# Kernel optimization log

Measured on AMD Instinct MI355X. Metric: run time of the kernel, lower is better.

Reference implementation:

```python
import jax, jax.numpy as jnp
import numpy as np

B, E = 8, 4096  # batch, embedding_size


def setup_inputs() -> dict:
    key = jax.random.key(0)
    k0, k1, k2, k3, k4 = jax.random.split(key, 5)
    return {
        "input": jax.random.normal(k0, (B, E), dtype=jnp.float32),
        "yin": jax.random.normal(k1, (B, E), dtype=jnp.float32),
        "hebb": jax.random.normal(k2, (E, E), dtype=jnp.float32),
        # learned parameters (match torch init: 0.01*randn / 0.01*ones)
        "w": 0.01 * jax.random.normal(k3, (E, E), dtype=jnp.float32),
        "alpha": 0.01 * jax.random.normal(k4, (E, E), dtype=jnp.float32),
        "eta": 0.01 * jnp.ones((1,), dtype=jnp.float32),
    }


def reference(input, yin, hebb, w, alpha, eta):
    # hebbian plasticity forward:
    # yout = tanh(yin @ (w + alpha * hebb) + input)            [B, E]
    yout = jnp.tanh(yin @ (w + alpha * hebb) + input)
    # hebb' = (1 - eta) * hebb + eta * outer(yin[0], yout[0])  [E, E]
    # (torch code does bmm(yin.unsqueeze(2), yout.unsqueeze(1))[0] -> batch-0 outer product)
    hebb_new = (1.0 - eta) * hebb + eta * jnp.outer(yin[0], yout[0])
    return yout, hebb_new
```

## Files before the change

### kernel.cpp

```cpp
#include <hip/hip_runtime.h>
#include <math.h>

#define E      4096
#define BATCH  8
#define COLB   256
#define KB     128
#define NCOLB  (E / COLB)
#define NKB    (E / KB)

typedef float f32x4 __attribute__((ext_vector_type(4)));

__global__ __launch_bounds__(256) void partial_gemm_kernel(
    const float* __restrict__ yin,
    const float* __restrict__ hebb,
    const float* __restrict__ w,
    const float* __restrict__ alpha,
    float* __restrict__ partial)
{
    __shared__ __align__(16) float s_yin[BATCH * KB];
    __shared__ __align__(16) float s_red[4 * BATCH * COLB];

    const int t    = threadIdx.x;
    const int lane = t & 63;
    const int wave = t >> 6;
    const int colBlock = blockIdx.x;
    const int kBlock   = blockIdx.y;

    {
        const int b   = t >> 5;
        const int off = (t & 31) * 4;
        const float4 v = *reinterpret_cast<const float4*>(
            yin + (size_t)b * E + (size_t)kBlock * KB + off);
        *reinterpret_cast<float4*>(&s_yin[b * KB + off]) = v;
    }
    __syncthreads();

    const int col0 = colBlock * COLB + lane * 4;

    float4 acc[BATCH];
#pragma unroll
    for (int b = 0; b < BATCH; ++b) acc[b] = make_float4(0.f, 0.f, 0.f, 0.f);

    const int kLocal0 = wave * (KB / 4);

#pragma unroll 2
    for (int kk = 0; kk < KB / 4; ++kk) {
        const int kL = kLocal0 + kk;
        const size_t row = (size_t)(kBlock * KB + kL) * E + col0;

        const float4 w4 = *reinterpret_cast<const float4*>(w + row);
        const float4 a4 = *reinterpret_cast<const float4*>(alpha + row);
        const float4 h4 = *reinterpret_cast<const float4*>(hebb + row);

        float4 m;
        m.x = w4.x + a4.x * h4.x;
        m.y = w4.y + a4.y * h4.y;
        m.z = w4.z + a4.z * h4.z;
        m.w = w4.w + a4.w * h4.w;

#pragma unroll
        for (int b = 0; b < BATCH; ++b) {
            const float yv = s_yin[b * KB + kL];
            acc[b].x = fmaf(yv, m.x, acc[b].x);
            acc[b].y = fmaf(yv, m.y, acc[b].y);
            acc[b].z = fmaf(yv, m.z, acc[b].z);
            acc[b].w = fmaf(yv, m.w, acc[b].w);
        }
    }

#pragma unroll
    for (int b = 0; b < BATCH; ++b) {
        *reinterpret_cast<float4*>(&s_red[(wave * BATCH + b) * COLB + lane * 4]) = acc[b];
    }
    __syncthreads();

#pragma unroll
    for (int b = 0; b < BATCH; ++b) {
        const int col = t;
        const float s = s_red[(0 * BATCH + b) * COLB + col]
                      + s_red[(1 * BATCH + b) * COLB + col]
                      + s_red[(2 * BATCH + b) * COLB + col]
                      + s_red[(3 * BATCH + b) * COLB + col];
        partial[((size_t)kBlock * BATCH + b) * E + colBlock * COLB + col] = s;
    }
}

__global__ __launch_bounds__(256) void finalize_yout_kernel(
    const float* __restrict__ input,
    const float* __restrict__ partial,
    float* __restrict__ yout)
{
    const int idx = blockIdx.x * 256 + threadIdx.x;
    const int b = idx >> 12;
    const int j = idx & (E - 1);

    float s = input[idx];
#pragma unroll
    for (int kb = 0; kb < NKB; ++kb)
        s += partial[((size_t)kb * BATCH + b) * E + j];

    yout[idx] = tanhf(s);
}

__global__ __launch_bounds__(256) void hebb_update_kernel(
    const float* __restrict__ hebb,
    const float* __restrict__ yin,
    const float* __restrict__ yout,
    const float* __restrict__ eta_p,
    float* __restrict__ hebb_out)
{
    const float eta  = eta_p[0];
    const float keep = 1.0f - eta;

    const size_t N4 = (size_t)E * E / 4;
    const size_t stride = (size_t)gridDim.x * blockDim.x;

    for (size_t i4 = (size_t)blockIdx.x * blockDim.x + threadIdx.x; i4 < N4; i4 += stride) {
        const size_t base = i4 * 4;
        const int row = (int)(base >> 12);
        const int jcol = (int)(base & (E - 1));

        const float y0 = yin[row] * eta;
        const float4 h  = *reinterpret_cast<const float4*>(hebb + base);
        const float4 yo = *reinterpret_cast<const float4*>(yout + jcol);

        f32x4 r;
        r.x = fmaf(y0, yo.x, keep * h.x);
        r.y = fmaf(y0, yo.y, keep * h.y);
        r.z = fmaf(y0, yo.z, keep * h.z);
        r.w = fmaf(y0, yo.w, keep * h.w);

        __builtin_nontemporal_store(r, reinterpret_cast<f32x4*>(hebb_out + base));
    }
}

extern "C" void kernel_launch(void* const* d_in, const int* in_sizes, int n_in,
                              void* d_out, int out_size, void* d_ws, size_t ws_size,
                              hipStream_t stream) {
    const float* input = (const float*)d_in[0];
    const float* yin   = (const float*)d_in[1];
    const float* hebb  = (const float*)d_in[2];
    const float* w     = (const float*)d_in[3];
    const float* alpha = (const float*)d_in[4];
    const float* eta   = (const float*)d_in[5];

    float* out      = (float*)d_out;
    float* yout     = out;
    float* hebb_out = out + (size_t)BATCH * E;
    float* partial  = (float*)d_ws;

    dim3 gridA(NCOLB, NKB);
    partial_gemm_kernel<<<gridA, 256, 0, stream>>>(yin, hebb, w, alpha, partial);

    finalize_yout_kernel<<<(BATCH * E) / 256, 256, 0, stream>>>(input, partial, yout);

    hebb_update_kernel<<<2048, 256, 0, stream>>>(hebb, yin, yout, eta, hebb_out);
}
```

Baseline: 58.78 us.

## Fuse yout finalization into the hebb update kernel with per-stripe recompute

Merges the finalize and hebb-update kernels into one 2D-grid kernel. Each block recomputes the batch-0 yout for its 128-column stripe from the split-K partials and keeps it in shared memory. Blocks in row chunk 0 also write the full yout for their stripe. This removes one kernel launch and the dependency on a global yout round trip. The cost is redundant reduction work: each of the 64 row-chunk blocks per stripe re-reads 32 partials per column, and the rc==0 blocks carry extra load that can leave the grid imbalanced.

```diff
diff --git a/kernel.cpp b/kernel.cpp
--- a/kernel.cpp
+++ b/kernel.cpp
@@ -85,52 +85,70 @@
     }
 }
 
-__global__ __launch_bounds__(256) void finalize_yout_kernel(
+#define STRIPE 128
+#define RCHUNK 64
+
+__global__ __launch_bounds__(256) void fused_bc_kernel(
     const float* __restrict__ input,
     const float* __restrict__ partial,
-    float* __restrict__ yout)
-{
-    const int idx = blockIdx.x * 256 + threadIdx.x;
-    const int b = idx >> 12;
-    const int j = idx & (E - 1);
-
-    float s = input[idx];
-#pragma unroll
-    for (int kb = 0; kb < NKB; ++kb)
-        s += partial[((size_t)kb * BATCH + b) * E + j];
-
-    yout[idx] = tanhf(s);
-}
-
-__global__ __launch_bounds__(256) void hebb_update_kernel(
+    const float* __restrict__ yin,
     const float* __restrict__ hebb,
-    const float* __restrict__ yin,
-    const float* __restrict__ yout,
     const float* __restrict__ eta_p,
+    float* __restrict__ yout,
     float* __restrict__ hebb_out)
 {
+    const int cs = blockIdx.x;
+    const int rc = blockIdx.y;
+    const int t  = threadIdx.x;
+    const int col0 = cs * STRIPE;
+
+    __shared__ __align__(16) float s_y0[STRIPE];
+
+    if (t < STRIPE) {
+        const int j = col0 + t;
+        float s = input[j];
+#pragma unroll 8
+        for (int kb = 0; kb < NKB; ++kb)
+            s += partial[((size_t)kb * BATCH + 0) * E + j];
+        s_y0[t] = tanhf(s);
+    }
+
+    if (rc == 0) {
+        for (int i = t; i < BATCH * STRIPE; i += 256) {
+            const int b = i >> 7;
+            const int j = col0 + (i & (STRIPE - 1));
+            float s = input[(size_t)b * E + j];
+#pragma unroll 8
+            for (int kb = 0; kb < NKB; ++kb)
+                s += partial[((size_t)kb * BATCH + b) * E + j];
+            yout[(size_t)b * E + j] = tanhf(s);
+        }
+    }
+    __syncthreads();
+
     const float eta  = eta_p[0];
     const float keep = 1.0f - eta;
 
-    const size_t N4 = (size_t)E * E / 4;
-    const size_t stride = (size_t)gridDim.x * blockDim.x;
+    const int cq = (t & 31) * 4;
+    const int rbase = rc * RCHUNK + (t >> 5);
 
-    for (size_t i4 = (size_t)blockIdx.x * blockDim.x + threadIdx.x; i4 < N4; i4 += stride) {
-        const size_t base = i4 * 4;
-        const int row = (int)(base >> 12);
-        const int jcol = (int)(base & (E - 1));
+    const float4 yo = *reinterpret_cast<const float4*>(&s_y0[cq]);
 
+#pragma unroll
+    for (int r = 0; r < 8; ++r) {
+        const int row = rbase + r * 8;
+        const size_t base = (size_t)row * E + col0 + cq;
         const float y0 = yin[row] * eta;
-        const float4 h  = *reinterpret_cast<const float4*>(hebb + base);
-        const float4 yo = *reinterpret_cast<const float4*>(yout + jcol);
 
-        f32x4 r;
-        r.x = fmaf(y0, yo.x, keep * h.x);
-        r.y = fmaf(y0, yo.y, keep * h.y);
-        r.z = fmaf(y0, yo.z, keep * h.z);
-        r.w = fmaf(y0, yo.w, keep * h.w);
+        const float4 h = *reinterpret_cast<const float4*>(hebb + base);
 
-        __builtin_nontemporal_store(r, reinterpret_cast<f32x4*>(hebb_out + base));
+        f32x4 o;
+        o.x = fmaf(y0, yo.x, keep * h.x);
+        o.y = fmaf(y0, yo.y, keep * h.y);
+        o.z = fmaf(y0, yo.z, keep * h.z);
+        o.w = fmaf(y0, yo.w, keep * h.w);
+
+        __builtin_nontemporal_store(o, reinterpret_cast<f32x4*>(hebb_out + base));
     }
 }
 
@@ -152,7 +170,7 @@
     dim3 gridA(NCOLB, NKB);
     partial_gemm_kernel<<<gridA, 256, 0, stream>>>(yin, hebb, w, alpha, partial);
 
-    finalize_yout_kernel<<<(BATCH * E) / 256, 256, 0, stream>>>(input, partial, yout);
-
-    hebb_update_kernel<<<2048, 256, 0, stream>>>(hebb, yin, yout, eta, hebb_out);
+    dim3 gridBC(E / STRIPE, E / RCHUNK);
+    fused_bc_kernel<<<gridBC, 256, 0, stream>>>(input, partial, yin, hebb, eta,
+                                                yout, hebb_out);
 }
```

Measured after the change: 59.65 us. About the same (+1.5%).
